# Performance work log

Hardware: AMD Instinct MI355X
Metric: run time of the kernel (lower is better)

The kernel has to match this reference:

```python
import jax, jax.numpy as jnp
import numpy as np

B, N, IN_DIM, HEADS, PER_HEAD = 8, 512, 256, 4, 32
OUT_DIM = HEADS * PER_HEAD  # 128
NEG_SLOPE = 0.2


def setup_inputs() -> dict:
    key = jax.random.key(0)
    ks = jax.random.split(key, 8)
    x = jax.random.normal(ks[0], (B, N, IN_DIM), jnp.float32)
    adj = jax.random.randint(ks[1], (B, N, N), 0, 2, jnp.int32)
    sl = 1.0 / np.sqrt(IN_DIM)
    W_l = jax.random.normal(ks[2], (IN_DIM, OUT_DIM), jnp.float32) * sl  # source proj
    b_l = jnp.zeros((OUT_DIM,), jnp.float32)
    W_r = jax.random.normal(ks[3], (IN_DIM, OUT_DIM), jnp.float32) * sl  # target proj
    b_r = jnp.zeros((OUT_DIM,), jnp.float32)
    att = jax.random.normal(ks[4], (HEADS, PER_HEAD), jnp.float32) * (1.0 / np.sqrt(PER_HEAD))
    bias = jnp.zeros((OUT_DIM,), jnp.float32)
    return {"x": x, "adj": adj, "W_l": W_l, "b_l": b_l, "W_r": W_r, "b_r": b_r,
            "att": att, "bias": bias}


def _gatv2_single(x_b, adj_b, W_l, b_l, W_r, b_r, att, bias):
    # PyG GATv2Conv: remove_self_loops + add_self_loops -> diagonal forced to 1
    n = x_b.shape[0]
    adj_sl = jnp.fill_diagonal(adj_b, 1, inplace=False)
    # edge_index = adj.nonzero().t(): source = row, target = col
    m = (adj_sl != 0).T  # m[i, j]: source j feeds target i
    xl = (x_b @ W_l + b_l).reshape(n, HEADS, PER_HEAD)  # source-side features
    xr = (x_b @ W_r + b_r).reshape(n, HEADS, PER_HEAD)  # target-side features
    s = xr[:, None] + xl[None, :]                       # [i, j, H, C]
    s = jnp.where(s > 0, s, NEG_SLOPE * s)              # LeakyReLU(0.2)
    e = jnp.einsum('ijhc,hc->ijh', s, att)              # attention logits
    e = jnp.where(m[..., None], e, -jnp.inf)
    alpha = jax.nn.softmax(e, axis=1)                   # softmax over sources j
    out = jnp.einsum('ijh,jhc->ihc', alpha, xl).reshape(n, HEADS * PER_HEAD)
    return out + bias


def reference(x, adj, W_l, b_l, W_r, b_r, att, bias):
    # Sequential per-batch processing, faithful to the original Python loop
    # and keeping the [N,N,H,C] intermediate to one graph at a time.
    def one(args):
        x_b, adj_b = args
        return _gatv2_single(x_b, adj_b, W_l, b_l, W_r, b_r, att, bias)
    return jax.lax.map(one, (x, adj))  # [B, N, OUT_DIM]
```

## Files before the change

kernel.cpp:

```cpp
#include <hip/hip_runtime.h>
#include <hip/hip_bf16.h>

#define B_   8
#define N_   512
#define IND  256
#define H_   4
#define PH   32
#define OD   128
#define TI   2

typedef float v2f __attribute__((ext_vector_type(2)));

#define ATT_SCALE 0.5770780163555854f
#define DLR_SCALE 0.8656170245333781f

template <int PAT>
__device__ __forceinline__ float dpp_add(float x) {
    int yi = __builtin_amdgcn_mov_dpp(__float_as_int(x), PAT, 0xF, 0xF, true);
    return x + __int_as_float(yi);
}

__device__ __forceinline__ float fast_exp2(float x) {
#if __has_builtin(__builtin_amdgcn_exp2f)
    return __builtin_amdgcn_exp2f(x);
#else
    return exp2f(x);
#endif
}

__device__ __forceinline__ void pk_fma(v2f& d, v2f a, v2f b) {
    asm("v_pk_fma_f32 %0, %1, %2, %0" : "+v"(d) : "v"(a), "v"(b));
}

__global__ __launch_bounds__(256, 2) void proj_kernel(
    const float* __restrict__ x,
    const float* __restrict__ Wl, const float* __restrict__ bl,
    const float* __restrict__ Wr, const float* __restrict__ br,
    const float* __restrict__ att,
    float* __restrict__ xl, float* __restrict__ xr,
    float* __restrict__ dl, float* __restrict__ dr)
{
    __shared__ float xs[8 * IND];
    const int t = threadIdx.x;
    const int row0 = blockIdx.x * 8;

    const float4* xp4 = (const float4*)(x + (size_t)row0 * IND);
    float4* xs4 = (float4*)xs;
    #pragma unroll
    for (int k = 0; k < 2; ++k)
        xs4[t + k * 256] = xp4[t + k * 256];
    __syncthreads();

    const int which = t >> 7;
    const int rg = (t >> 6) & 1;
    const int og = t & 63;
    const int o0 = og * 2;
    const int r0 = rg * 4;
    const float* W  = which ? Wr : Wl;
    const float* bb = which ? br : bl;

    float acc0[4], acc1[4];
    #pragma unroll
    for (int r = 0; r < 4; ++r) { acc0[r] = 0.f; acc1[r] = 0.f; }

    for (int k = 0; k < IND; k += 4) {
        float wf0[4], wf1[4];
        #pragma unroll
        for (int kk = 0; kk < 4; ++kk) {
            float2 wv = *(const float2*)(W + (size_t)(k + kk) * OD + o0);
            wf0[kk] = wv.x;
            wf1[kk] = wv.y;
        }
        float xv[4][4];
        #pragma unroll
        for (int r = 0; r < 4; ++r)
            *(float4*)(xv[r]) = *(const float4*)(&xs[(r0 + r) * IND + k]);
        #pragma unroll
        for (int kk = 0; kk < 4; ++kk)
            #pragma unroll
            for (int r = 0; r < 4; ++r) {
                acc0[r] = fmaf(xv[r][kk], wf0[kk], acc0[r]);
                acc1[r] = fmaf(xv[r][kk], wf1[kk], acc1[r]);
            }
    }

    const float bv0 = bb[o0];
    const float bv1 = bb[o0 + 1];
    const float a0 = att[o0];
    const float a1 = att[o0 + 1];
    float* dst = which ? xr : xl;
    float* dp  = which ? dr : dl;
    float dcon[4];
    #pragma unroll
    for (int r = 0; r < 4; ++r) {
        float y0 = acc0[r] + bv0;
        float y1 = acc1[r] + bv1;
        *(float2*)(&dst[(size_t)(row0 + r0 + r) * OD + o0]) = make_float2(y0, y1);
        dcon[r] = fmaf(a0, y0, a1 * y1);
    }
    #pragma unroll
    for (int m = 1; m < 16; m <<= 1) {
        #pragma unroll
        for (int r = 0; r < 4; ++r)
            dcon[r] += __shfl_xor(dcon[r], m);
    }
    if ((og & 15) == 0) {
        const int h = og >> 4;
        #pragma unroll
        for (int r = 0; r < 4; ++r)
            dp[(size_t)(row0 + r0 + r) * H_ + h] = DLR_SCALE * dcon[r];
    }
}

__global__ __launch_bounds__(256, 3) void attn_kernel(
    const int* __restrict__ adj, const float* __restrict__ att,
    const float* __restrict__ bias,
    const float* __restrict__ xl, const float* __restrict__ xr,
    const float* __restrict__ dl, const float* __restrict__ dr,
    float* __restrict__ out)
{
    const int t = threadIdx.x;
    const int b  = blockIdx.x >> 8;
    const int i0 = (blockIdx.x & 255) * TI;
    const int cq = t & 3;
    const int js = (t >> 2) & 15;
    const int h  = t >> 6;
    const int cbase = h * PH + cq * 8;

    float atS[8];
    {
        const float* ap = att + cbase;
        float4 a0 = *(const float4*)(ap);
        float4 a1 = *(const float4*)(ap + 4);
        atS[0] = ATT_SCALE * a0.x; atS[1] = ATT_SCALE * a0.y;
        atS[2] = ATT_SCALE * a0.z; atS[3] = ATT_SCALE * a0.w;
        atS[4] = ATT_SCALE * a1.x; atS[5] = ATT_SCALE * a1.y;
        atS[6] = ATT_SCALE * a1.z; atS[7] = ATT_SCALE * a1.w;
    }
    float xrS[TI][8];
    float drv[TI];
    #pragma unroll
    for (int il = 0; il < TI; ++il) {
        const float* xp = xr + ((size_t)(b * N_ + i0 + il)) * OD + cbase;
        float4 r0 = *(const float4*)(xp);
        float4 r1 = *(const float4*)(xp + 4);
        xrS[il][0] = r0.x; xrS[il][1] = r0.y; xrS[il][2] = r0.z; xrS[il][3] = r0.w;
        xrS[il][4] = r1.x; xrS[il][5] = r1.y; xrS[il][6] = r1.z; xrS[il][7] = r1.w;
        drv[il] = dr[((size_t)(b * N_ + i0 + il)) * H_ + h];
    }

    v2f acc[TI][4];
    float sumw[TI];
    #pragma unroll
    for (int il = 0; il < TI; ++il) {
        sumw[il] = 0.f;
        #pragma unroll
        for (int m = 0; m < 4; ++m) acc[il][m] = (v2f){0.f, 0.f};
    }

    const float* xlp = xl + ((size_t)(b * N_ + js)) * OD + cbase;
    const int*   ajp = adj + ((size_t)(b * N_ + js)) * N_ + i0;
    const float* dlp = dl + ((size_t)(b * N_ + js)) * H_ + h;

    float4 va = *(const float4*)(xlp);
    float4 vb = *(const float4*)(xlp + 4);
    int2   mj = *(const int2*)(ajp);
    float  dj = *dlp;

    #pragma unroll 2
    for (int u = 0; u < 32; ++u) {
        float4 wa = va, wb = vb;
        int2   wm = mj;
        float  wd = dj;
        if (u < 31) {
            xlp += 16 * OD; ajp += 16 * N_; dlp += 16 * H_;
            va = *(const float4*)(xlp);
            vb = *(const float4*)(xlp + 4);
            mj = *(const int2*)(ajp);
            dj = *dlp;
        }
        const int j = u * 16 + js;
        v2f p0 = (v2f){wa.x, wa.y}, p1 = (v2f){wa.z, wa.w};
        v2f p2 = (v2f){wb.x, wb.y}, p3 = (v2f){wb.z, wb.w};
        int wmv[TI] = {wm.x, wm.y};
        #pragma unroll
        for (int il = 0; il < TI; ++il) {
            float s, e2a = 0.f, e2b = 0.f;
            s = xrS[il][0] + wa.x; e2a = fmaf(atS[0], __builtin_fabsf(s), e2a);
            s = xrS[il][1] + wa.y; e2b = fmaf(atS[1], __builtin_fabsf(s), e2b);
            s = xrS[il][2] + wa.z; e2a = fmaf(atS[2], __builtin_fabsf(s), e2a);
            s = xrS[il][3] + wa.w; e2b = fmaf(atS[3], __builtin_fabsf(s), e2b);
            s = xrS[il][4] + wb.x; e2a = fmaf(atS[4], __builtin_fabsf(s), e2a);
            s = xrS[il][5] + wb.y; e2b = fmaf(atS[5], __builtin_fabsf(s), e2b);
            s = xrS[il][6] + wb.z; e2a = fmaf(atS[6], __builtin_fabsf(s), e2a);
            s = xrS[il][7] + wb.w; e2b = fmaf(atS[7], __builtin_fabsf(s), e2b);
            float eh = e2a + e2b;
            eh = dpp_add<0xB1>(eh);
            eh = dpp_add<0x4E>(eh);
            float e = (wd + drv[il]) + eh;
            bool keep = (wmv[il] != 0) || (j == i0 + il);
            float w = keep ? fast_exp2(e) : 0.f;
            sumw[il] += w;
            v2f ws = (v2f){w, w};
            pk_fma(acc[il][0], ws, p0);
            pk_fma(acc[il][1], ws, p1);
            pk_fma(acc[il][2], ws, p2);
            pk_fma(acc[il][3], ws, p3);
        }
    }

    #pragma unroll
    for (int il = 0; il < TI; ++il) {
        sumw[il] += __shfl_xor(sumw[il], 4);
        sumw[il] += __shfl_xor(sumw[il], 8);
        sumw[il] += __shfl_xor(sumw[il], 16);
        sumw[il] += __shfl_xor(sumw[il], 32);
    }

    float accf[16];
    #pragma unroll
    for (int il = 0; il < TI; ++il)
        #pragma unroll
        for (int m = 0; m < 4; ++m) {
            accf[il * 8 + 2 * m]     = acc[il][m].x;
            accf[il * 8 + 2 * m + 1] = acc[il][m].y;
        }

    float r8[8];
    {
        const bool hi = (js & 1) != 0;
        #pragma unroll
        for (int m = 0; m < 8; ++m) {
            float send = hi ? accf[m] : accf[8 + m];
            float keep = hi ? accf[8 + m] : accf[m];
            r8[m] = keep + __shfl_xor(send, 4);
        }
    }
    float r4[4];
    {
        const bool hi = (js & 2) != 0;
        #pragma unroll
        for (int m = 0; m < 4; ++m) {
            float send = hi ? r8[m] : r8[4 + m];
            float keep = hi ? r8[4 + m] : r8[m];
            r4[m] = keep + __shfl_xor(send, 8);
        }
    }
    float r2[2];
    {
        const bool hi = (js & 4) != 0;
        #pragma unroll
        for (int m = 0; m < 2; ++m) {
            float send = hi ? r4[m] : r4[2 + m];
            float keep = hi ? r4[2 + m] : r4[m];
            r2[m] = keep + __shfl_xor(send, 16);
        }
    }
    float r1;
    {
        const bool hi = (js & 8) != 0;
        float send = hi ? r2[0] : r2[1];
        float keep = hi ? r2[1] : r2[0];
        r1 = keep + __shfl_xor(send, 32);
    }

    const int il = js & 1;
    const int coff = ((js >> 1) & 1) * 4 + ((js >> 2) & 1) * 2 + ((js >> 3) & 1);
    const int c = cbase + coff;
    const float inv = 1.f / sumw[il];
    out[((size_t)(b * N_ + i0 + il)) * OD + c] = fmaf(r1, inv, bias[c]);
}

extern "C" void kernel_launch(void* const* d_in, const int* in_sizes, int n_in,
                              void* d_out, int out_size, void* d_ws, size_t ws_size,
                              hipStream_t stream) {
    const float* x    = (const float*)d_in[0];
    const int*   adj  = (const int*)d_in[1];
    const float* Wl   = (const float*)d_in[2];
    const float* bl   = (const float*)d_in[3];
    const float* Wr   = (const float*)d_in[4];
    const float* br   = (const float*)d_in[5];
    const float* att  = (const float*)d_in[6];
    const float* bias = (const float*)d_in[7];
    float* out = (float*)d_out;

    float* xl = (float*)d_ws;
    float* xr = xl + (size_t)B_ * N_ * OD;
    float* dl = xr + (size_t)B_ * N_ * OD;
    float* dr = dl + (size_t)B_ * N_ * H_;

    proj_kernel<<<512, 256, 0, stream>>>(x, Wl, bl, Wr, br, att, xl, xr, dl, dr);
    attn_kernel<<<2048, 256, 0, stream>>>(adj, att, bias, xl, xr, dl, dr, out);
}
```

Before: 130.4 us.

## Process four target rows per block and use packed adds for scores

```diff
diff --git a/kernel.cpp b/kernel.cpp
--- a/kernel.cpp
+++ b/kernel.cpp
@@ -7,7 +7,7 @@
 #define H_   4
 #define PH   32
 #define OD   128
-#define TI   2
+#define TI   4
 
 typedef float v2f __attribute__((ext_vector_type(2)));
 
@@ -30,6 +30,11 @@
 
 __device__ __forceinline__ void pk_fma(v2f& d, v2f a, v2f b) {
     asm("v_pk_fma_f32 %0, %1, %2, %0" : "+v"(d) : "v"(a), "v"(b));
+}
+__device__ __forceinline__ v2f pk_add(v2f a, v2f b) {
+    v2f d;
+    asm("v_pk_add_f32 %0, %1, %2" : "=v"(d) : "v"(a), "v"(b));
+    return d;
 }
 
 __global__ __launch_bounds__(256, 2) void proj_kernel(
@@ -120,8 +125,8 @@
     float* __restrict__ out)
 {
     const int t = threadIdx.x;
-    const int b  = blockIdx.x >> 8;
-    const int i0 = (blockIdx.x & 255) * TI;
+    const int b  = blockIdx.x >> 7;
+    const int i0 = (blockIdx.x & 127) * TI;
     const int cq = t & 3;
     const int js = (t >> 2) & 15;
     const int h  = t >> 6;
@@ -137,15 +142,17 @@
         atS[4] = ATT_SCALE * a1.x; atS[5] = ATT_SCALE * a1.y;
         atS[6] = ATT_SCALE * a1.z; atS[7] = ATT_SCALE * a1.w;
     }
-    float xrS[TI][8];
+    v2f xr2[TI][4];
     float drv[TI];
     #pragma unroll
     for (int il = 0; il < TI; ++il) {
         const float* xp = xr + ((size_t)(b * N_ + i0 + il)) * OD + cbase;
         float4 r0 = *(const float4*)(xp);
         float4 r1 = *(const float4*)(xp + 4);
-        xrS[il][0] = r0.x; xrS[il][1] = r0.y; xrS[il][2] = r0.z; xrS[il][3] = r0.w;
-        xrS[il][4] = r1.x; xrS[il][5] = r1.y; xrS[il][6] = r1.z; xrS[il][7] = r1.w;
+        xr2[il][0] = (v2f){r0.x, r0.y};
+        xr2[il][1] = (v2f){r0.z, r0.w};
+        xr2[il][2] = (v2f){r1.x, r1.y};
+        xr2[il][3] = (v2f){r1.z, r1.w};
         drv[il] = dr[((size_t)(b * N_ + i0 + il)) * H_ + h];
     }
 
@@ -164,36 +171,41 @@
 
     float4 va = *(const float4*)(xlp);
     float4 vb = *(const float4*)(xlp + 4);
-    int2   mj = *(const int2*)(ajp);
+    int4   mj = *(const int4*)(ajp);
     float  dj = *dlp;
 
     #pragma unroll 2
     for (int u = 0; u < 32; ++u) {
         float4 wa = va, wb = vb;
-        int2   wm = mj;
+        int4   wm = mj;
         float  wd = dj;
         if (u < 31) {
             xlp += 16 * OD; ajp += 16 * N_; dlp += 16 * H_;
             va = *(const float4*)(xlp);
             vb = *(const float4*)(xlp + 4);
-            mj = *(const int2*)(ajp);
+            mj = *(const int4*)(ajp);
             dj = *dlp;
         }
         const int j = u * 16 + js;
         v2f p0 = (v2f){wa.x, wa.y}, p1 = (v2f){wa.z, wa.w};
         v2f p2 = (v2f){wb.x, wb.y}, p3 = (v2f){wb.z, wb.w};
-        int wmv[TI] = {wm.x, wm.y};
+        int wmv[TI] = {wm.x, wm.y, wm.z, wm.w};
         #pragma unroll
         for (int il = 0; il < TI; ++il) {
-            float s, e2a = 0.f, e2b = 0.f;
-            s = xrS[il][0] + wa.x; e2a = fmaf(atS[0], __builtin_fabsf(s), e2a);
-            s = xrS[il][1] + wa.y; e2b = fmaf(atS[1], __builtin_fabsf(s), e2b);
-            s = xrS[il][2] + wa.z; e2a = fmaf(atS[2], __builtin_fabsf(s), e2a);
-            s = xrS[il][3] + wa.w; e2b = fmaf(atS[3], __builtin_fabsf(s), e2b);
-            s = xrS[il][4] + wb.x; e2a = fmaf(atS[4], __builtin_fabsf(s), e2a);
-            s = xrS[il][5] + wb.y; e2b = fmaf(atS[5], __builtin_fabsf(s), e2b);
-            s = xrS[il][6] + wb.z; e2a = fmaf(atS[6], __builtin_fabsf(s), e2a);
-            s = xrS[il][7] + wb.w; e2b = fmaf(atS[7], __builtin_fabsf(s), e2b);
+            float e2a = 0.f, e2b = 0.f;
+            v2f s;
+            s = pk_add(xr2[il][0], p0);
+            e2a = fmaf(atS[0], __builtin_fabsf(s.x), e2a);
+            e2b = fmaf(atS[1], __builtin_fabsf(s.y), e2b);
+            s = pk_add(xr2[il][1], p1);
+            e2a = fmaf(atS[2], __builtin_fabsf(s.x), e2a);
+            e2b = fmaf(atS[3], __builtin_fabsf(s.y), e2b);
+            s = pk_add(xr2[il][2], p2);
+            e2a = fmaf(atS[4], __builtin_fabsf(s.x), e2a);
+            e2b = fmaf(atS[5], __builtin_fabsf(s.y), e2b);
+            s = pk_add(xr2[il][3], p3);
+            e2a = fmaf(atS[6], __builtin_fabsf(s.x), e2a);
+            e2b = fmaf(atS[7], __builtin_fabsf(s.y), e2b);
             float eh = e2a + e2b;
             eh = dpp_add<0xB1>(eh);
             eh = dpp_add<0x4E>(eh);
@@ -217,7 +229,7 @@
         sumw[il] += __shfl_xor(sumw[il], 32);
     }
 
-    float accf[16];
+    float accf[32];
     #pragma unroll
     for (int il = 0; il < TI; ++il)
         #pragma unroll
@@ -226,49 +238,56 @@
             accf[il * 8 + 2 * m + 1] = acc[il][m].y;
         }
 
+    float r16[16];
+    {
+        const bool hi = (js & 1) != 0;
+        #pragma unroll
+        for (int m = 0; m < 16; ++m) {
+            float send = hi ? accf[m] : accf[16 + m];
+            float keep = hi ? accf[16 + m] : accf[m];
+            r16[m] = keep + __shfl_xor(send, 4);
+        }
+    }
     float r8[8];
     {
-        const bool hi = (js & 1) != 0;
+        const bool hi = (js & 2) != 0;
         #pragma unroll
         for (int m = 0; m < 8; ++m) {
-            float send = hi ? accf[m] : accf[8 + m];
-            float keep = hi ? accf[8 + m] : accf[m];
-            r8[m] = keep + __shfl_xor(send, 4);
+            float send = hi ? r16[m] : r16[8 + m];
+            float keep = hi ? r16[8 + m] : r16[m];
+            r8[m] = keep + __shfl_xor(send, 8);
         }
     }
     float r4[4];
     {
-        const bool hi = (js & 2) != 0;
+        const bool hi = (js & 4) != 0;
         #pragma unroll
         for (int m = 0; m < 4; ++m) {
             float send = hi ? r8[m] : r8[4 + m];
             float keep = hi ? r8[4 + m] : r8[m];
-            r4[m] = keep + __shfl_xor(send, 8);
+            r4[m] = keep + __shfl_xor(send, 16);
         }
     }
     float r2[2];
     {
-        const bool hi = (js & 4) != 0;
+        const bool hi = (js & 8) != 0;
         #pragma unroll
         for (int m = 0; m < 2; ++m) {
             float send = hi ? r4[m] : r4[2 + m];
             float keep = hi ? r4[2 + m] : r4[m];
-            r2[m] = keep + __shfl_xor(send, 16);
-        }
-    }
-    float r1;
-    {
-        const bool hi = (js & 8) != 0;
-        float send = hi ? r2[0] : r2[1];
-        float keep = hi ? r2[1] : r2[0];
-        r1 = keep + __shfl_xor(send, 32);
-    }
-
-    const int il = js & 1;
-    const int coff = ((js >> 1) & 1) * 4 + ((js >> 2) & 1) * 2 + ((js >> 3) & 1);
+            r2[m] = keep + __shfl_xor(send, 32);
+        }
+    }
+
+    const int il = ((js & 1) << 1) | ((js >> 1) & 1);
+    const int coff = ((js >> 2) & 1) * 4 + ((js >> 3) & 1) * 2;
     const int c = cbase + coff;
-    const float inv = 1.f / sumw[il];
-    out[((size_t)(b * N_ + i0 + il)) * OD + c] = fmaf(r1, inv, bias[c]);
+    const float sw0 = (js & 1) ? ((js & 2) ? sumw[3] : sumw[2])
+                               : ((js & 2) ? sumw[1] : sumw[0]);
+    const float inv = 1.f / sw0;
+    float* op = out + ((size_t)(b * N_ + i0 + il)) * OD;
+    *(float2*)(&op[c]) = make_float2(fmaf(r2[0], inv, bias[c]),
+                                     fmaf(r2[1], inv, bias[c + 1]));
 }
 
 extern "C" void kernel_launch(void* const* d_in, const int* in_sizes, int n_in,
@@ -290,5 +309,5 @@
     float* dr = dl + (size_t)B_ * N_ * H_;
 
     proj_kernel<<<512, 256, 0, stream>>>(x, Wl, bl, Wr, br, att, xl, xr, dl, dr);
-    attn_kernel<<<2048, 256, 0, stream>>>(adj, att, bias, xl, xr, dl, dr, out);
-}
+    attn_kernel<<<1024, 256, 0, stream>>>(adj, att, bias, xl, xr, dl, dr, out);
+}
```

Result: faster. 122.9 us (-5.7%).
